# Optimization experiments

Hardware: AMD Instinct MI355X
Metric: run time of the kernel (lower is better)

Reference implementation:

```python
import jax, jax.numpy as jnp
import numpy as np

B, L, DIM = 2, 2048, 1024
H, DH, W = 16, 64, 256  # heads, head_dim, window_size
ROPE_BASE = 10000.0


def _rope(x):
    # x: [b, l, h, d] -> rotate consecutive pairs (torch view_as_complex semantics)
    l, d = x.shape[1], x.shape[3]
    freqs = 1.0 / (ROPE_BASE ** (jnp.arange(0, d, 2, dtype=jnp.float32) / d))  # [d/2]
    ang = jnp.arange(l, dtype=jnp.float32)[:, None] * freqs[None, :]           # [l, d/2]
    cos = jnp.cos(ang)[None, :, None, :].astype(x.dtype)
    sin = jnp.sin(ang)[None, :, None, :].astype(x.dtype)
    xe, xo = x[..., 0::2], x[..., 1::2]
    ye = xe * cos - xo * sin
    yo = xe * sin + xo * cos
    return jnp.stack([ye, yo], axis=-1).reshape(x.shape)


def setup_inputs() -> dict:
    key = jax.random.key(0)
    ks = jax.random.split(key, 7)
    sh = (B, L, DIM)
    return {
        "q": jax.random.normal(ks[0], sh, jnp.float32),
        "k": jax.random.normal(ks[1], sh, jnp.float32),
        "v": jax.random.normal(ks[2], sh, jnp.float32),
        "wq": jax.random.normal(ks[3], (H * DH, DIM), jnp.float32) * 0.02,
        "wk": jax.random.normal(ks[4], (H * DH, DIM), jnp.float32) * 0.02,
        "wv": jax.random.normal(ks[5], (H * DH, DIM), jnp.float32) * 0.02,
        "wo": jax.random.normal(ks[6], (DIM, H * DH), jnp.float32) * 0.02,
    }


def reference(q, k, v, wq, wk, wv, wo):
    b, l, _ = q.shape
    qh = (q @ wq.T).reshape(b, l, H, DH)
    kh = (k @ wk.T).reshape(b, l, H, DH)
    vh = (v @ wv.T).reshape(b, l, H, DH).transpose(0, 2, 1, 3)  # [b,h,l,d]
    qh = _rope(qh).transpose(0, 2, 1, 3)                        # [b,h,l,d]
    kh = _rope(kh).transpose(0, 2, 1, 3)
    scores = jnp.einsum('bhqd,bhkd->bhqk', qh, kh) * (DH ** -0.5)
    i = jnp.arange(l)[:, None]
    j = jnp.arange(l)[None, :]
    window_mask = (j <= i) & (j >= i - W)  # keys in [i-W, i], matches the loop
    scores = jnp.where(window_mask, scores, -1e30)
    probs = jax.nn.softmax(scores, axis=-1)
    out = jnp.einsum('bhqk,bhkd->bhqd', probs, vh)
    out = out.transpose(0, 2, 1, 3).reshape(b, l, H * DH)
    return out @ wo.T
```

## Files before the change

kernel.cpp:

```cpp
#include <hip/hip_runtime.h>
#include <stdint.h>

#define B_    2
#define L_    2048
#define DIM_  1024
#define H_    16
#define DH_   64
#define WWIN  256

typedef __attribute__((ext_vector_type(4))) float f32x4;
typedef __attribute__((ext_vector_type(8))) short bf16x8;

__device__ __forceinline__ unsigned short f2bf(float x) {
  union { float f; unsigned u; } c; c.f = x;
  unsigned r = c.u + 0x7fffu + ((c.u >> 16) & 1u);
  return (unsigned short)(r >> 16);
}

struct CastArgs {
  const float* src[7];
  unsigned short* dst[7];
};
__global__ __launch_bounds__(256) void cast_bf16_kernel(CastArgs a) {
  int bid = blockIdx.x;
  int arr, base;
  if (bid < 12288) {
    arr = bid >> 12;
    base = (bid & 4095) << 10;
  } else {
    int t = bid - 12288;
    arr = 3 + (t >> 10);
    base = (t & 1023) << 10;
  }
  int i = base + (int)threadIdx.x * 4;
  float4 v = *(const float4*)(a.src[arr] + i);
  ushort4 o;
  o.x = f2bf(v.x); o.y = f2bf(v.y); o.z = f2bf(v.z); o.w = f2bf(v.w);
  *(ushort4*)(a.dst[arr] + i) = o;
}

#define BM 128

__device__ __forceinline__ void gld_lds16(const void* g, void* l) {
  __builtin_amdgcn_global_load_lds(
      (const __attribute__((address_space(1))) void*)g,
      (__attribute__((address_space(3))) void*)l, 16, 0, 0);
}

__device__ __forceinline__ void gemm_core_128x128(
    const unsigned short* __restrict__ A, const unsigned short* __restrict__ Bt,
    unsigned short* As, unsigned short* Bs, f32x4 (&acc)[4][4],
    int m0, int n0) {
  const int tid = threadIdx.x;
  const int wave = tid >> 6, lane = tid & 63;
  const int quad = lane >> 4, l16 = lane & 15;
  const int wm = wave >> 1, wn = wave & 1;
  const int srow = tid >> 3, sc = tid & 7;

  auto stage = [&](int k0, int buf) {
    unsigned short* Ad = As + buf * 8192;
    unsigned short* Bd = Bs + buf * 8192;
    #pragma unroll
    for (int rd = 0; rd < 4; ++rd) {
      int row = rd * 32 + srow;
      int cs = sc ^ (row & 7);
      gld_lds16(A + (size_t)(m0 + row) * 1024 + k0 + cs * 8, Ad + row * 64 + sc * 8);
    }
    #pragma unroll
    for (int rd = 0; rd < 4; ++rd) {
      int row = rd * 32 + srow;
      int cs = sc ^ (row & 7);
      gld_lds16(Bt + (size_t)(n0 + row) * 1024 + k0 + cs * 8, Bd + row * 64 + sc * 8);
    }
  };

  stage(0, 0);
  for (int k = 0; k < 16; ++k) {
    const int cur = k & 1;
    __syncthreads();
    if (k < 15) stage((k + 1) * 64, cur ^ 1);
    const unsigned short* Ac = As + cur * 8192;
    const unsigned short* Bc = Bs + cur * 8192;
    #pragma unroll
    for (int ks = 0; ks < 2; ++ks) {
      bf16x8 af[4], bfr[4];
      #pragma unroll
      for (int i = 0; i < 4; ++i) {
        int row = wm * 64 + i * 16 + l16;
        int ch = (ks * 4 + quad) ^ (row & 7);
        af[i] = *(const bf16x8*)(Ac + row * 64 + ch * 8);
      }
      #pragma unroll
      for (int j = 0; j < 4; ++j) {
        int row = wn * 64 + j * 16 + l16;
        int ch = (ks * 4 + quad) ^ (row & 7);
        bfr[j] = *(const bf16x8*)(Bc + row * 64 + ch * 8);
      }
      #pragma unroll
      for (int i = 0; i < 4; ++i)
        #pragma unroll
        for (int j = 0; j < 4; ++j)
          acc[i][j] = __builtin_amdgcn_mfma_f32_16x16x32_bf16(af[i], bfr[j], acc[i][j], 0, 0, 0);
    }
  }
}

struct ProjArgs {
  const unsigned short* A[3];
  const unsigned short* Bt[3];
  unsigned short* C[3];
};
__global__ __launch_bounds__(256) void gemm_proj_kernel(ProjArgs pa) {
  __shared__ unsigned short SH[32768];
  unsigned short* As = SH;
  unsigned short* Bs = SH + 16384;

  const int bflat = blockIdx.x;
  const int xcd = bflat & 7, s = bflat >> 3;
  const int nblk = s & 7;
  const int mz = xcd * 12 + (s >> 3);
  const int z = mz >> 5;
  const int mblk = mz & 31;
  const int m0 = mblk * BM, n0 = nblk * 128;

  f32x4 acc[4][4] = {};
  gemm_core_128x128(pa.A[z], pa.Bt[z], As, Bs, acc, m0, n0);

  const int tid = threadIdx.x;
  const int lane = tid & 63, wave = tid >> 6;
  const int quad = lane >> 4, l16 = lane & 15;
  const int wm = wave >> 1, wn = wave & 1;
  const int h = nblk * 2 + wn;

  if (z < 2) {
    float frev[4];
    #pragma unroll
    for (int j = 0; j < 4; ++j) {
      int d = j * 16 + l16;
      frev[j] = exp2f(-(float)(d >> 1) * 0.41524101186092029f) * 0.15915494309189535f;
    }
    unsigned short* C = pa.C[z];
    const bool even = (l16 & 1) == 0;
    #pragma unroll
    for (int i = 0; i < 4; ++i)
      #pragma unroll
      for (int r = 0; r < 4; ++r) {
        int m = m0 + wm * 64 + i * 16 + quad * 4 + r;
        int b = m >> 11, l = m & (L_ - 1);
        float lf = (float)l;
        #pragma unroll
        for (int j = 0; j < 4; ++j) {
          int d = j * 16 + l16;
          float v = acc[i][j][r];
          float p = __shfl_xor(v, 1);
          float a = lf * frev[j];
          float t = a - floorf(a);
          float sn = __builtin_amdgcn_sinf(t);
          float cs = __builtin_amdgcn_cosf(t);
          float o = even ? (v * cs - p * sn) : (p * sn + v * cs);
          C[(((size_t)b * H_ + h) * L_ + l) * DH_ + d] = f2bf(o);
        }
      }
  } else {
    __syncthreads();
    char* T = (char*)SH + wave * 8192;
    #pragma unroll
    for (int i = 0; i < 4; ++i)
      #pragma unroll
      for (int j = 0; j < 4; ++j) {
        int d = j * 16 + l16;
        int mb = i * 32 + quad * 8;
        int ch = mb >> 4, sub = mb & 15;
        uint2 pk;
        pk.x = (unsigned)f2bf(acc[i][j][0]) | ((unsigned)f2bf(acc[i][j][1]) << 16);
        pk.y = (unsigned)f2bf(acc[i][j][2]) | ((unsigned)f2bf(acc[i][j][3]) << 16);
        *(uint2*)(T + d * 128 + ((ch ^ (d & 7)) << 4) + sub) = pk;
      }
    asm volatile("s_waitcnt lgkmcnt(0)" ::: "memory");
    int b = m0 >> 11;
    int lbase = (m0 & (L_ - 1)) + wm * 64;
    unsigned short* C = pa.C[2];
    #pragma unroll
    for (int t = 0; t < 8; ++t) {
      int d = t * 8 + (lane >> 3);
      int ch = lane & 7;
      uint4 o = *(uint4*)(T + d * 128 + ((ch ^ (d & 7)) << 4));
      *(uint4*)(C + (((size_t)b * H_ + h) * DH_ + d) * L_ + lbase + ch * 8) = o;
    }
  }
}

__global__ __launch_bounds__(256) void gemm_out_kernel(
    const unsigned short* __restrict__ A, const unsigned short* __restrict__ Bt,
    float* __restrict__ C) {
  __shared__ unsigned short SH[32768];
  unsigned short* As = SH;
  unsigned short* Bs = SH + 16384;

  const int bflat = blockIdx.x;
  const int xcd = bflat & 7, s = bflat >> 3;
  const int nblk = s & 7;
  const int mblk = xcd * 4 + (s >> 3);
  const int m0 = mblk * BM, n0 = nblk * 128;

  f32x4 acc[4][4] = {};
  gemm_core_128x128(A, Bt, As, Bs, acc, m0, n0);

  const int lane = threadIdx.x & 63, wave = threadIdx.x >> 6;
  const int quad = lane >> 4, l16 = lane & 15;
  const int wm = wave >> 1, wn = wave & 1;
  #pragma unroll
  for (int i = 0; i < 4; ++i)
    #pragma unroll
    for (int j = 0; j < 4; ++j)
      #pragma unroll
      for (int r = 0; r < 4; ++r) {
        int m = m0 + wm * 64 + i * 16 + quad * 4 + r;
        int n = n0 + wn * 64 + j * 16 + l16;
        C[(size_t)m * DIM_ + n] = acc[i][j][r];
      }
}

#define PSTR 292
__global__ __launch_bounds__(256) void attn_kernel(
    const unsigned short* __restrict__ Qh,
    const unsigned short* __restrict__ Kh,
    const unsigned short* __restrict__ Vt,
    unsigned short* __restrict__ O) {
  __shared__ unsigned short Ps[4][16 * PSTR];
  const int tid = threadIdx.x;
  const int wave = tid >> 6, lane = tid & 63;
  const int quad = lane >> 4, l16 = lane & 15;

  const int bflat = blockIdx.x;
  const int xcd = bflat & 7, s = bflat >> 3;
  const int qt = s >> 2;
  const int bh = xcd * 4 + (s & 3);

  const int qb = qt * 64 + wave * 16;
  const int kw0 = qb - WWIN;
  const bool edge = (kw0 < 0);

  unsigned short* pw = &Ps[wave][0];
  #pragma unroll
  for (int r = 0; r < 4; ++r)
    pw[(quad * 4 + r) * PSTR + 272 + l16] = 0;

  bf16x8 qf0, qf1;
  {
    const unsigned short* qrow = Qh + ((size_t)bh * L_ + qb + l16) * DH_;
    qf0 = *(const bf16x8*)(qrow + quad * 8);
    qf1 = *(const bf16x8*)(qrow + 32 + quad * 8);
  }

  f32x4 S[17] = {};
  const unsigned short* kbase = Kh + (size_t)bh * L_ * DH_;
  #pragma unroll
  for (int c = 0; c < 17; ++c) {
    int key = kw0 + c * 16 + l16;
    key = key < 0 ? 0 : key;
    const unsigned short* kr = kbase + (size_t)key * DH_ + quad * 8;
    bf16x8 kf0 = *(const bf16x8*)(kr);
    bf16x8 kf1 = *(const bf16x8*)(kr + 32);
    S[c] = __builtin_amdgcn_mfma_f32_16x16x32_bf16(qf0, kf0, S[c], 0, 0, 0);
    S[c] = __builtin_amdgcn_mfma_f32_16x16x32_bf16(qf1, kf1, S[c], 0, 0, 0);
  }

  float inv_l[4];
  #pragma unroll
  for (int r = 0; r < 4; ++r) {
    const int qr = quad * 4 + r;
    const int i = qb + qr;
    float mx = -1e30f;
    #pragma unroll
    for (int c = 0; c < 17; ++c) {
      float v = S[c][r];
      if (c == 0 || c == 16 || edge) {
        int key = kw0 + c * 16 + l16;
        bool valid = (key >= 0) && (key <= i) && (key >= i - WWIN);
        v = valid ? v : -1e30f;
        S[c][r] = v;
      }
      mx = fmaxf(mx, v);
    }
    mx = fmaxf(mx, __shfl_xor(mx, 1));
    mx = fmaxf(mx, __shfl_xor(mx, 2));
    mx = fmaxf(mx, __shfl_xor(mx, 4));
    mx = fmaxf(mx, __shfl_xor(mx, 8));
    float sum = 0.f;
    #pragma unroll
    for (int c = 0; c < 17; ++c) {
      float e = __builtin_amdgcn_exp2f((S[c][r] - mx) * 0.18033688011112042f);
      S[c][r] = e;
      sum += e;
    }
    sum += __shfl_xor(sum, 1);
    sum += __shfl_xor(sum, 2);
    sum += __shfl_xor(sum, 4);
    sum += __shfl_xor(sum, 8);
    inv_l[r] = 1.0f / sum;
  }

  #pragma unroll
  for (int c = 0; c < 17; ++c)
    #pragma unroll
    for (int r = 0; r < 4; ++r)
      pw[(quad * 4 + r) * PSTR + c * 16 + l16] = f2bf(S[c][r] * inv_l[r]);
  asm volatile("s_waitcnt lgkmcnt(0)" ::: "memory");

  f32x4 Oacc[4] = {};
  const unsigned short* vbase = Vt + (size_t)bh * DH_ * L_;
  #pragma unroll
  for (int g = 0; g < 9; ++g) {
    bf16x8 pf = *(const bf16x8*)(pw + l16 * PSTR + g * 32 + quad * 8);
    int vk = kw0 + g * 32 + quad * 8;
    vk = vk < 0 ? 0 : vk;
    vk = vk > (L_ - 8) ? (L_ - 8) : vk;
    #pragma unroll
    for (int t = 0; t < 4; ++t) {
      bf16x8 vf = *(const bf16x8*)(vbase + (size_t)(t * 16 + l16) * L_ + vk);
      Oacc[t] = __builtin_amdgcn_mfma_f32_16x16x32_bf16(pf, vf, Oacc[t], 0, 0, 0);
    }
  }

  int b = bh >> 4, h = bh & 15;
  #pragma unroll
  for (int t = 0; t < 4; ++t)
    #pragma unroll
    for (int r = 0; r < 4; ++r) {
      int l = qb + quad * 4 + r;
      int col = h * DH_ + t * 16 + l16;
      O[((size_t)b * L_ + l) * (H_ * DH_) + col] = f2bf(Oacc[t][r]);
    }
}

extern "C" void kernel_launch(void* const* d_in, const int* in_sizes, int n_in,
                              void* d_out, int out_size, void* d_ws, size_t ws_size,
                              hipStream_t stream) {
  const float* q  = (const float*)d_in[0];
  const float* k  = (const float*)d_in[1];
  const float* v  = (const float*)d_in[2];
  const float* wq = (const float*)d_in[3];
  const float* wk = (const float*)d_in[4];
  const float* wv = (const float*)d_in[5];
  const float* wo = (const float*)d_in[6];

  const size_t SA = (size_t)B_ * L_ * DIM_;
  const size_t SW = (size_t)DIM_ * DIM_;
  unsigned short* w   = (unsigned short*)d_ws;
  unsigned short* qb  = w; w += SA;
  unsigned short* kb  = w; w += SA;
  unsigned short* vb  = w; w += SA;
  unsigned short* wqb = w; w += SW;
  unsigned short* wkb = w; w += SW;
  unsigned short* wvb = w; w += SW;
  unsigned short* wob = w; w += SW;
  unsigned short* qh  = w; w += SA;
  unsigned short* kh  = w; w += SA;
  unsigned short* vt  = w; w += SA;
  unsigned short* Ob  = w; w += SA;

  CastArgs ca;
  ca.src[0] = q;  ca.dst[0] = qb;
  ca.src[1] = k;  ca.dst[1] = kb;
  ca.src[2] = v;  ca.dst[2] = vb;
  ca.src[3] = wq; ca.dst[3] = wqb;
  ca.src[4] = wk; ca.dst[4] = wkb;
  ca.src[5] = wv; ca.dst[5] = wvb;
  ca.src[6] = wo; ca.dst[6] = wob;
  cast_bf16_kernel<<<dim3(16384), 256, 0, stream>>>(ca);

  ProjArgs pa;
  pa.A[0] = qb; pa.Bt[0] = wqb; pa.C[0] = qh;
  pa.A[1] = kb; pa.Bt[1] = wkb; pa.C[1] = kh;
  pa.A[2] = vb; pa.Bt[2] = wvb; pa.C[2] = vt;
  gemm_proj_kernel<<<dim3(768), 256, 0, stream>>>(pa);

  attn_kernel<<<dim3(32 * 32), 256, 0, stream>>>(qh, kh, vt, Ob);
  gemm_out_kernel<<<dim3(256), 256, 0, stream>>>(Ob, wob, (float*)d_out);
}
```

Baseline: 207.6 us.

## Stage V window in shared memory and pass P via lane shuffles

The attention kernel now loads the block's 64x320 V-transpose window into LDS once, shared by all four waves, instead of each wave reading V from global memory. QK^T is computed transposed (K as the A operand), so each lane holds a single query's scores and softmax reductions shrink to two cross-lane shuffles. Probabilities are packed with v_cvt_pk_bf16_f32 and moved into the PV operand layout with lane shuffles rather than a round trip through per-wave LDS. A block barrier and the occupancy hint of 3 blocks per CU are added, which constrains register allocation.

```diff
diff --git a/kernel.cpp b/kernel.cpp
--- a/kernel.cpp
+++ b/kernel.cpp
@@ -221,13 +221,13 @@
       }
 }
 
-#define PSTR 292
-__global__ __launch_bounds__(256) void attn_kernel(
+#define VSTR 344
+__global__ __launch_bounds__(256, 3) void attn_kernel(
     const unsigned short* __restrict__ Qh,
     const unsigned short* __restrict__ Kh,
     const unsigned short* __restrict__ Vt,
     unsigned short* __restrict__ O) {
-  __shared__ unsigned short Ps[4][16 * PSTR];
+  __shared__ unsigned short Vs[64 * VSTR];
   const int tid = threadIdx.x;
   const int wave = tid >> 6, lane = tid & 63;
   const int quad = lane >> 4, l16 = lane & 15;
@@ -237,14 +237,30 @@
   const int qt = s >> 2;
   const int bh = xcd * 4 + (s & 3);
 
-  const int qb = qt * 64 + wave * 16;
+  const int q0 = qt * 64;
+  const int qb = q0 + wave * 16;
   const int kw0 = qb - WWIN;
   const bool edge = (kw0 < 0);
 
-  unsigned short* pw = &Ps[wave][0];
-  #pragma unroll
-  for (int r = 0; r < 4; ++r)
-    pw[(quad * 4 + r) * PSTR + 272 + l16] = 0;
+  const unsigned short* vbase = Vt + (size_t)bh * DH_ * L_;
+  uint4 vstage[11];
+  #pragma unroll
+  for (int it = 0; it < 11; ++it) {
+    int ci = it * 256 + tid;
+    int row = ci / 42, ch = ci - row * 42;
+    int key0 = q0 - WWIN + ch * 8;
+    key0 = key0 < 0 ? 0 : key0;
+    key0 = key0 > (L_ - 8) ? (L_ - 8) : key0;
+    if (ci < 2688)
+      vstage[it] = *(const uint4*)(vbase + (size_t)row * L_ + key0);
+  }
+  #pragma unroll
+  for (int it = 0; it < 11; ++it) {
+    int ci = it * 256 + tid;
+    int row = ci / 42, ch = ci - row * 42;
+    if (ci < 2688)
+      *(uint4*)(&Vs[row * VSTR + ch * 8]) = vstage[it];
+  }
 
   bf16x8 qf0, qf1;
   {
@@ -262,64 +278,82 @@
     const unsigned short* kr = kbase + (size_t)key * DH_ + quad * 8;
     bf16x8 kf0 = *(const bf16x8*)(kr);
     bf16x8 kf1 = *(const bf16x8*)(kr + 32);
-    S[c] = __builtin_amdgcn_mfma_f32_16x16x32_bf16(qf0, kf0, S[c], 0, 0, 0);
-    S[c] = __builtin_amdgcn_mfma_f32_16x16x32_bf16(qf1, kf1, S[c], 0, 0, 0);
-  }
-
-  float inv_l[4];
+    S[c] = __builtin_amdgcn_mfma_f32_16x16x32_bf16(kf0, qf0, S[c], 0, 0, 0);
+    S[c] = __builtin_amdgcn_mfma_f32_16x16x32_bf16(kf1, qf1, S[c], 0, 0, 0);
+  }
+
+  const int off16 = quad * 4;
   #pragma unroll
   for (int r = 0; r < 4; ++r) {
-    const int qr = quad * 4 + r;
-    const int i = qb + qr;
-    float mx = -1e30f;
-    #pragma unroll
-    for (int c = 0; c < 17; ++c) {
-      float v = S[c][r];
-      if (c == 0 || c == 16 || edge) {
-        int key = kw0 + c * 16 + l16;
-        bool valid = (key >= 0) && (key <= i) && (key >= i - WWIN);
-        v = valid ? v : -1e30f;
-        S[c][r] = v;
-      }
-      mx = fmaxf(mx, v);
-    }
-    mx = fmaxf(mx, __shfl_xor(mx, 1));
-    mx = fmaxf(mx, __shfl_xor(mx, 2));
-    mx = fmaxf(mx, __shfl_xor(mx, 4));
-    mx = fmaxf(mx, __shfl_xor(mx, 8));
-    float sum = 0.f;
-    #pragma unroll
-    for (int c = 0; c < 17; ++c) {
+    if (off16 + r < l16)  S[0][r]  = -1e30f;
+    if (off16 + r > l16)  S[16][r] = -1e30f;
+  }
+  if (edge) {
+    #pragma unroll
+    for (int c = 0; c < 17; ++c)
+      #pragma unroll
+      for (int r = 0; r < 4; ++r)
+        if (kw0 + c * 16 + off16 + r < 0) S[c][r] = -1e30f;
+  }
+
+  float mx = -1e30f;
+  #pragma unroll
+  for (int c = 0; c < 17; ++c)
+    #pragma unroll
+    for (int r = 0; r < 4; ++r)
+      mx = fmaxf(mx, S[c][r]);
+  mx = fmaxf(mx, __shfl_xor(mx, 16));
+  mx = fmaxf(mx, __shfl_xor(mx, 32));
+  float sum = 0.f;
+  #pragma unroll
+  for (int c = 0; c < 17; ++c)
+    #pragma unroll
+    for (int r = 0; r < 4; ++r) {
       float e = __builtin_amdgcn_exp2f((S[c][r] - mx) * 0.18033688011112042f);
       S[c][r] = e;
       sum += e;
     }
-    sum += __shfl_xor(sum, 1);
-    sum += __shfl_xor(sum, 2);
-    sum += __shfl_xor(sum, 4);
-    sum += __shfl_xor(sum, 8);
-    inv_l[r] = 1.0f / sum;
-  }
-
-  #pragma unroll
-  for (int c = 0; c < 17; ++c)
-    #pragma unroll
-    for (int r = 0; r < 4; ++r)
-      pw[(quad * 4 + r) * PSTR + c * 16 + l16] = f2bf(S[c][r] * inv_l[r]);
-  asm volatile("s_waitcnt lgkmcnt(0)" ::: "memory");
+  sum += __shfl_xor(sum, 16);
+  sum += __shfl_xor(sum, 32);
+  const float ivl = 1.0f / sum;
+
+  __syncthreads();
 
   f32x4 Oacc[4] = {};
-  const unsigned short* vbase = Vt + (size_t)bh * DH_ * L_;
+  const int srcA = (lane & 15) | ((lane & 16) << 1);
+  const int srcB = srcA + 16;
+  const bool loq = quad < 2;
   #pragma unroll
   for (int g = 0; g < 9; ++g) {
-    bf16x8 pf = *(const bf16x8*)(pw + l16 * PSTR + g * 32 + quad * 8);
-    int vk = kw0 + g * 32 + quad * 8;
-    vk = vk < 0 ? 0 : vk;
-    vk = vk > (L_ - 8) ? (L_ - 8) : vk;
+    unsigned uA0, uA1, uB0, uB1;
+    {
+      float a0 = S[2 * g][0] * ivl, a1 = S[2 * g][1] * ivl;
+      float a2 = S[2 * g][2] * ivl, a3 = S[2 * g][3] * ivl;
+      asm("v_cvt_pk_bf16_f32 %0, %1, %2" : "=v"(uA0) : "v"(a0), "v"(a1));
+      asm("v_cvt_pk_bf16_f32 %0, %1, %2" : "=v"(uA1) : "v"(a2), "v"(a3));
+    }
+    if (g < 8) {
+      float b0 = S[2 * g + 1][0] * ivl, b1 = S[2 * g + 1][1] * ivl;
+      float b2 = S[2 * g + 1][2] * ivl, b3 = S[2 * g + 1][3] * ivl;
+      asm("v_cvt_pk_bf16_f32 %0, %1, %2" : "=v"(uB0) : "v"(b0), "v"(b1));
+      asm("v_cvt_pk_bf16_f32 %0, %1, %2" : "=v"(uB1) : "v"(b2), "v"(b3));
+    } else {
+      uB0 = 0; uB1 = 0;
+    }
+    unsigned tA0a = __shfl(uA0, srcA), tA1a = __shfl(uA1, srcA);
+    unsigned tB0a = __shfl(uB0, srcA), tB1a = __shfl(uB1, srcA);
+    unsigned tA0b = __shfl(uA0, srcB), tA1b = __shfl(uA1, srcB);
+    unsigned tB0b = __shfl(uB0, srcB), tB1b = __shfl(uB1, srcB);
+    union { unsigned u[4]; bf16x8 v; } pa;
+    pa.u[0] = loq ? tA0a : tB0a;
+    pa.u[1] = loq ? tA1a : tB1a;
+    pa.u[2] = loq ? tA0b : tB0b;
+    pa.u[3] = loq ? tA1b : tB1b;
+    const int kloc = wave * 16 + g * 32 + quad * 8;
     #pragma unroll
     for (int t = 0; t < 4; ++t) {
-      bf16x8 vf = *(const bf16x8*)(vbase + (size_t)(t * 16 + l16) * L_ + vk);
-      Oacc[t] = __builtin_amdgcn_mfma_f32_16x16x32_bf16(pf, vf, Oacc[t], 0, 0, 0);
+      bf16x8 vf = *(const bf16x8*)(&Vs[(t * 16 + l16) * VSTR + kloc]);
+      Oacc[t] = __builtin_amdgcn_mfma_f32_16x16x32_bf16(pa.v, vf, Oacc[t], 0, 0, 0);
     }
   }
 
```

New measurement: 213.0 us. +2.6%, slower.
